# Performance work log

Hardware: AMD Instinct MI355X
Metric: run time of the kernel (lower is better)

The kernel has to match this reference:

```python
import jax, jax.numpy as jnp
import numpy as np

B, T, IN, H = 256, 512, 256, 1024


def setup_inputs() -> dict:
    key = jax.random.key(0)
    ks = jax.random.split(key, 11)
    bound = 1.0 / np.sqrt(H)  # PyTorch nn.RNN / nn.Linear init bound
    u = lambda k, shape: jax.random.uniform(k, shape, jnp.float32, -bound, bound)
    return {
        "y0": jax.random.normal(ks[0], (B, IN), jnp.float32),
        "t": jnp.arange(T, dtype=jnp.float32),
        "W_ih0": u(ks[1], (H, IN)),
        "W_hh0": u(ks[2], (H, H)),
        "b_ih0": u(ks[3], (H,)),
        "b_hh0": u(ks[4], (H,)),
        "W_ih1": u(ks[5], (H, H)),
        "W_hh1": u(ks[6], (H, H)),
        "b_ih1": u(ks[7], (H,)),
        "b_hh1": u(ks[8], (H,)),
        "fc_W": u(ks[9], (IN, H)),
        "fc_b": u(ks[10], (IN,)),
    }


def reference(y0, t, W_ih0, W_hh0, b_ih0, b_hh0, W_ih1, W_hh1, b_ih1, b_hh1, fc_W, fc_b):
    b = y0.shape[0]
    h = W_hh0.shape[0]
    n_steps = t.shape[0] - 1  # static under jit
    h0 = jnp.zeros((b, h), y0.dtype)
    h1 = jnp.zeros((b, h), y0.dtype)

    def step(carry, _):
        h0, h1, y = carry
        h0n = jnp.tanh(y @ W_ih0.T + b_ih0 + h0 @ W_hh0.T + b_hh0)
        h1n = jnp.tanh(h0n @ W_ih1.T + b_ih1 + h1 @ W_hh1.T + b_hh1)
        yn = h1n @ fc_W.T + fc_b  # fed back as next input
        return (h0n, h1n, yn), yn

    _, ys = jax.lax.scan(step, (h0, h1, y0), None, length=n_steps)  # [T-1, B, IN]
    out = jnp.concatenate([y0[None], ys], axis=0)  # [T, B, IN]
    return jnp.transpose(out, (1, 0, 2))  # [B, T, IN]
```

## Files before the change

kernel.cpp:

```cpp
#include <hip/hip_runtime.h>


#define B_SZ   256
#define IN_SZ  256
#define H_SZ   1024
#define KCAT   2048
#define NWG_M  64

typedef short v8s __attribute__((ext_vector_type(8)));
typedef float v4f __attribute__((ext_vector_type(4)));

__device__ __forceinline__ unsigned short bf16rne(float f) {
  unsigned x = __builtin_bit_cast(unsigned, f);
  return (unsigned short)((x + 0x7fffu + ((x >> 16) & 1u)) >> 16);
}
__device__ __forceinline__ float bf2f(unsigned short u) {
  unsigned x = ((unsigned)u) << 16;
  return __builtin_bit_cast(float, x);
}

__device__ __forceinline__ void split8(const float* __restrict__ p,
                                       v8s& a0, v8s& a1) {
  float4 x0 = *(const float4*)p;
  float4 x1 = *(const float4*)(p + 4);
  float v[8] = {x0.x, x0.y, x0.z, x0.w, x1.x, x1.y, x1.z, x1.w};
  v8s h, l;
#pragma unroll
  for (int j = 0; j < 8; ++j) {
    unsigned u = __builtin_bit_cast(unsigned, v[j]);
    float r = v[j] - __builtin_bit_cast(float, u & 0xFFFF0000u);
    h[j] = (short)(u >> 16);
    l[j] = (short)(__builtin_bit_cast(unsigned, r) >> 16);
  }
  a0 = h; a1 = l;
}

__device__ __forceinline__ void grid_barrier(unsigned* cnt, int idx, unsigned nwg,
                                             unsigned* abortf, unsigned* fail_s,
                                             bool* dead) {
  __syncthreads();
  if (*dead) return;
  if (threadIdx.x == 0) {
    __builtin_amdgcn_fence(__ATOMIC_RELEASE, "agent");
    __hip_atomic_fetch_add(&cnt[idx], 1u, __ATOMIC_RELAXED, __HIP_MEMORY_SCOPE_AGENT);
    unsigned f = 0, it = 0;
    while (__hip_atomic_load(&cnt[idx], __ATOMIC_RELAXED, __HIP_MEMORY_SCOPE_AGENT) < nwg) {
      __builtin_amdgcn_s_sleep(2);
      if ((++it & 1023u) == 0u) {
        if (__hip_atomic_load(abortf, __ATOMIC_RELAXED, __HIP_MEMORY_SCOPE_AGENT)) { f = 1; break; }
        if (it > 4000000u) {
          f = 1;
          __hip_atomic_store(abortf, 1u, __ATOMIC_RELAXED, __HIP_MEMORY_SCOPE_AGENT);
          break;
        }
      }
    }
    __builtin_amdgcn_fence(__ATOMIC_ACQUIRE, "agent");
    *fail_s = f;
  }
  __syncthreads();
  if (*fail_s) *dead = true;
}

struct MArgs {
  const float* y0;
  const unsigned short *B0p, *B1p, *W0p, *fcp;
  float *h0a, *h0b, *h1a, *h1b;
  const float *b_init, *b0p, *b1p, *fc_b;
  float* out;
  unsigned *cnt, *abortf;
  int T, nwg;
};

__device__ __forceinline__ void gemm2f(
    const float* __restrict__ X, int ldx, int am0, int ak0,
    const unsigned short* __restrict__ Bp, int KBtot, int bn0, int bk0,
    int ksteps, int l15, int l4, v4f acc[4][4]) {
  const float* Ab = X + (long)(am0 + l15) * ldx + ak0 + l4 * 8;
  const unsigned short* Bb =
      Bp + ((long)(bn0 + l15) * KBtot + (bk0 >> 3) + l4) * 16;
  for (int ks = 0; ks < ksteps; ++ks) {
    v8s a0[4], a1[4], b0[4], b1[4];
#pragma unroll
    for (int f = 0; f < 4; ++f) {
      split8(Ab + (long)f * 16 * ldx + ks * 32, a0[f], a1[f]);
      const unsigned short* bp = Bb + (long)f * 16 * KBtot * 16 + ks * 64;
      b0[f] = *(const v8s*)bp;
      b1[f] = *(const v8s*)(bp + 8);
    }
#pragma unroll
    for (int fr = 0; fr < 4; ++fr) {
#pragma unroll
      for (int fc = 0; fc < 4; ++fc) {
        v4f c = acc[fr][fc];
        c = __builtin_amdgcn_mfma_f32_16x16x32_bf16(a0[fr], b1[fc], c, 0, 0, 0);
        c = __builtin_amdgcn_mfma_f32_16x16x32_bf16(a1[fr], b0[fc], c, 0, 0, 0);
        c = __builtin_amdgcn_mfma_f32_16x16x32_bf16(a0[fr], b0[fc], c, 0, 0, 0);
        acc[fr][fc] = c;
      }
    }
  }
}

#define RSTRIDE 68

__global__ void __launch_bounds__(256, 1) rnn_mfma_kernel(MArgs a) {
  __shared__ float red[4][64 * RSTRIDE];
  __shared__ unsigned fail_s;
  bool dead = false;

  const int wg = blockIdx.x, tid = threadIdx.x;
  const int wv = tid >> 6, lane = tid & 63;
  const int l15 = lane & 15, l4 = lane >> 4;
  const int T = a.T, nwg = a.nwg;
  const long ldo = (long)T * IN_SZ;

  const int m0 = (wg >> 4) * 64;
  const int n0 = (wg & 15) * 64;
  const int fn0 = (wg & 15) * 16;

  float* h0p[2] = {a.h0a, a.h0b};
  float* h1p[2] = {a.h1a, a.h1b};

  v4f zero = {0.f, 0.f, 0.f, 0.f};
  int cur = 0, bar = 0;

  const int ak0 = 512 * (wv & 1);
  const int bk0 = ak0 + (wv >> 1) * 1024;

  for (int t = 1; t < T; ++t) {
    const int nxt = cur ^ 1;

    {
      v4f acc[4][4];
#pragma unroll
      for (int i = 0; i < 4; ++i)
#pragma unroll
        for (int j = 0; j < 4; ++j) acc[i][j] = zero;

      if (t == 1) {
        gemm2f(a.y0, IN_SZ, m0, 64 * wv, a.W0p, 32, n0, 64 * wv,
               2, l15, l4, acc);
      } else {
        const float* X = (wv < 2) ? h1p[cur] : h0p[cur];
        gemm2f(X, H_SZ, m0, ak0, a.B0p, 256, n0, bk0, 16, l15, l4, acc);
      }
      float* my = &red[wv][0];
#pragma unroll
      for (int fr = 0; fr < 4; ++fr)
#pragma unroll
        for (int fc = 0; fc < 4; ++fc)
#pragma unroll
          for (int j = 0; j < 4; ++j)
            my[(fr * 16 + l4 * 4 + j) * RSTRIDE + fc * 16 + l15] = acc[fr][fc][j];
      __syncthreads();
      const float* bias = (t == 1) ? a.b_init : a.b0p;
      float* dst = h0p[nxt];
#pragma unroll
      for (int i = 0; i < 16; ++i) {
        int idx = i * 256 + tid;
        int row = idx >> 6, col = idx & 63;
        int ro = row * RSTRIDE + col;
        float v = red[0][ro] + red[1][ro] + red[2][ro] + red[3][ro];
        dst[(long)(m0 + row) * H_SZ + n0 + col] = tanhf(v + bias[n0 + col]);
      }
    }
    grid_barrier(a.cnt, bar++, (unsigned)nwg, a.abortf, &fail_s, &dead);

    {
      v4f acc[4][4];
#pragma unroll
      for (int i = 0; i < 4; ++i)
#pragma unroll
        for (int j = 0; j < 4; ++j) acc[i][j] = zero;

      const float* X = (wv < 2) ? h0p[nxt] : h1p[cur];
      gemm2f(X, H_SZ, m0, ak0, a.B1p, 256, n0, bk0, 16, l15, l4, acc);

      float* my = &red[wv][0];
#pragma unroll
      for (int fr = 0; fr < 4; ++fr)
#pragma unroll
        for (int fc = 0; fc < 4; ++fc)
#pragma unroll
          for (int j = 0; j < 4; ++j)
            my[(fr * 16 + l4 * 4 + j) * RSTRIDE + fc * 16 + l15] = acc[fr][fc][j];
      __syncthreads();
      float* dst = h1p[nxt];
#pragma unroll
      for (int i = 0; i < 16; ++i) {
        int idx = i * 256 + tid;
        int row = idx >> 6, col = idx & 63;
        int ro = row * RSTRIDE + col;
        float v = red[0][ro] + red[1][ro] + red[2][ro] + red[3][ro];
        dst[(long)(m0 + row) * H_SZ + n0 + col] = tanhf(v + a.b1p[n0 + col]);
      }
    }
    grid_barrier(a.cnt, bar++, (unsigned)nwg, a.abortf, &fail_s, &dead);

    {
      v4f facc[4] = {zero, zero, zero, zero};
      const float* Ab = h1p[nxt] + (long)(m0 + l15) * H_SZ + 256 * wv + l4 * 8;
      const unsigned short* Bb =
          a.fcp + ((long)(fn0 + l15) * 128 + 32 * wv + l4) * 16;
      for (int ks = 0; ks < 8; ++ks) {
        const unsigned short* bp = Bb + ks * 64;
        v8s b0 = *(const v8s*)bp;
        v8s b1 = *(const v8s*)(bp + 8);
#pragma unroll
        for (int f = 0; f < 4; ++f) {
          v8s a0, a1;
          split8(Ab + (long)f * 16 * H_SZ + ks * 32, a0, a1);
          facc[f] = __builtin_amdgcn_mfma_f32_16x16x32_bf16(a0, b1, facc[f], 0, 0, 0);
          facc[f] = __builtin_amdgcn_mfma_f32_16x16x32_bf16(a1, b0, facc[f], 0, 0, 0);
          facc[f] = __builtin_amdgcn_mfma_f32_16x16x32_bf16(a0, b0, facc[f], 0, 0, 0);
        }
      }
      float* my = &red[wv][0];
#pragma unroll
      for (int f = 0; f < 4; ++f)
#pragma unroll
        for (int j = 0; j < 4; ++j)
          my[(f * 16 + l4 * 4 + j) * 17 + l15] = facc[f][j];
      __syncthreads();
#pragma unroll
      for (int i = 0; i < 4; ++i) {
        int idx = i * 256 + tid;
        int row = idx >> 4, col = idx & 15;
        int ro = row * 17 + col;
        float v = red[0][ro] + red[1][ro] + red[2][ro] + red[3][ro] + a.fc_b[fn0 + col];
        a.out[(long)(m0 + row) * ldo + (long)t * IN_SZ + fn0 + col] = v;
      }
      __syncthreads();
    }
    cur = nxt;
  }
}

__global__ void __launch_bounds__(256) pack2_kernel(
    const float* __restrict__ src, int R, int CB,
    unsigned short* __restrict__ dst, int KBtot, int kboff) {
  int i = blockIdx.x * 256 + threadIdx.x;
  if (i >= R * CB) return;
  int r = i / CB, cb = i - r * CB;
  const float* s = src + (long)r * (CB * 8) + cb * 8;
  unsigned short w[16];
#pragma unroll
  for (int e = 0; e < 8; ++e) {
    float v = s[e];
    unsigned short s0 = bf16rne(v);
    float rr = v - bf2f(s0);
    w[e] = s0;
    w[8 + e] = bf16rne(rr);
  }
  unsigned short* d = dst + ((long)r * KBtot + kboff + cb) * 16;
#pragma unroll
  for (int e = 0; e < 16; ++e) d[e] = w[e];
}

__global__ void __launch_bounds__(256) wc_pack2_kernel(
    const float* __restrict__ Wih0, const float* __restrict__ fcW,
    unsigned short* __restrict__ dst) {
  int i = blockIdx.x * 256 + threadIdx.x;
  int r = i >> 7, jb = i & 127;
  float acc[8] = {0.f, 0.f, 0.f, 0.f, 0.f, 0.f, 0.f, 0.f};
  for (int c = 0; c < IN_SZ; ++c) {
    float w = Wih0[r * IN_SZ + c];
    const float* f = &fcW[c * H_SZ + jb * 8];
#pragma unroll
    for (int e = 0; e < 8; ++e) acc[e] = fmaf(w, f[e], acc[e]);
  }
  unsigned short* d = dst + ((long)r * 256 + jb) * 16;
#pragma unroll
  for (int e = 0; e < 8; ++e) {
    unsigned short s0 = bf16rne(acc[e]);
    float rr = acc[e] - bf2f(s0);
    d[e] = s0;
    d[8 + e] = bf16rne(rr);
  }
}

__global__ void bias_kernel(const float* bih0, const float* bhh0,
                            const float* bih1, const float* bhh1,
                            const float* __restrict__ Wih0,
                            const float* __restrict__ fcb,
                            float* b_init, float* b0p, float* b1p) {
  int i = blockIdx.x * 256 + threadIdx.x;
  if (i < H_SZ) {
    float sum = 0.f;
    for (int c = 0; c < IN_SZ; ++c) sum += Wih0[i * IN_SZ + c] * fcb[c];
    float bi = bih0[i] + bhh0[i];
    b_init[i] = bi;
    b0p[i] = bi + sum;
    b1p[i] = bih1[i] + bhh1[i];
  }
}

__global__ void y0copy_kernel(const float* __restrict__ y0,
                              float* __restrict__ out, int T) {
  int o = blockIdx.x * 256 + threadIdx.x;
  int b = o >> 6, c = (o & 63) << 2;
  *(float4*)&out[(size_t)b * T * IN_SZ + c] = *(const float4*)&y0[b * IN_SZ + c];
}

#define KC 128
#define KCP 132
#define LTILES 256
#define FTILES 64
struct alignas(16) SmemT { float A[16][KCP]; float W[64][KCP]; };
struct RnnArgs {
  const float *y0, *W_ih0, *W_hh0, *W_ih1, *W_hh1, *fc_W, *fc_b;
  const float *Wc, *b_init, *b0p, *b1p;
  float *h0a, *h0b, *h1a, *h1b, *out;
  unsigned *cnt, *abortf;
  int T, nwg, mode;
};
__device__ __forceinline__ void gemm_accum(const float* __restrict__ X, int ldx,
                                           const float* __restrict__ Wm, int K,
                                           int m0, int n0, int wv, int lane, int tid,
                                           SmemT& s, float* acc) {
  for (int kc = 0; kc < K; kc += KC) {
#pragma unroll
    for (int i = 0; i < 2; ++i) {
      int a = i * 256 + tid; int r = a >> 5, k = (a & 31) << 2;
      *(float4*)&s.A[r][k] = *(const float4*)&X[(size_t)(m0 + r) * ldx + kc + k];
    }
#pragma unroll
    for (int i = 0; i < 8; ++i) {
      int a = i * 256 + tid; int c = a >> 5, k = (a & 31) << 2;
      *(float4*)&s.W[c][k] = *(const float4*)&Wm[(size_t)(n0 + c) * K + kc + k];
    }
    __syncthreads();
#pragma unroll 4
    for (int k4 = 0; k4 < KC; k4 += 4) {
      float4 w4 = *(float4*)&s.W[lane][k4];
#pragma unroll
      for (int j = 0; j < 4; ++j) {
        float4 a4 = *(float4*)&s.A[wv + 4 * j][k4];
        acc[j] = fmaf(a4.x, w4.x, acc[j]); acc[j] = fmaf(a4.y, w4.y, acc[j]);
        acc[j] = fmaf(a4.z, w4.z, acc[j]); acc[j] = fmaf(a4.w, w4.w, acc[j]);
      }
    }
    __syncthreads();
  }
}
__global__ void __launch_bounds__(256) rnn_seq_kernel(RnnArgs a) {
  __shared__ SmemT s;
  __shared__ unsigned fail_s;
  bool dead = false;
  const int wg = blockIdx.x, tid = threadIdx.x;
  const int wv = tid >> 6, lane = tid & 63;
  const int T = a.T, nwg = a.nwg, mode = a.mode;
  const int ldo = T * IN_SZ;
  const float* h0[2] = {a.h0a, a.h0b};
  const float* h1[2] = {a.h1a, a.h1b};
  float* h0w[2] = {a.h0a, a.h0b};
  float* h1w[2] = {a.h1a, a.h1b};
  int cur = 0, bar = 0;
  for (int t = 1; t < T; ++t) {
    const int nxt = cur ^ 1;
    for (int tl = wg; tl < LTILES; tl += nwg) {
      const int m0 = (tl >> 4) << 4;
      const int n0 = (((tl & 7) << 1) | ((tl >> 3) & 1)) << 6;
      float acc[4] = {0.f, 0.f, 0.f, 0.f};
      const float* bias;
      if (t == 1) { gemm_accum(a.y0, IN_SZ, a.W_ih0, IN_SZ, m0, n0, wv, lane, tid, s, acc); bias = a.b_init; }
      else if (mode == 0) { gemm_accum(h1[cur], H_SZ, a.Wc, H_SZ, m0, n0, wv, lane, tid, s, acc); bias = a.b0p; }
      else { gemm_accum(a.out + (size_t)(t - 1) * IN_SZ, ldo, a.W_ih0, IN_SZ, m0, n0, wv, lane, tid, s, acc); bias = a.b_init; }
      gemm_accum(h0[cur], H_SZ, a.W_hh0, H_SZ, m0, n0, wv, lane, tid, s, acc);
      const float bv = bias[n0 + lane];
#pragma unroll
      for (int j = 0; j < 4; ++j)
        h0w[nxt][(size_t)(m0 + wv + 4 * j) * H_SZ + n0 + lane] = tanhf(acc[j] + bv);
    }
    grid_barrier(a.cnt, bar++, (unsigned)nwg, a.abortf, &fail_s, &dead);
    for (int tl = wg; tl < LTILES; tl += nwg) {
      const int m0 = (tl >> 4) << 4;
      const int n0 = (((tl & 7) << 1) | ((tl >> 3) & 1)) << 6;
      float acc[4] = {0.f, 0.f, 0.f, 0.f};
      gemm_accum(h0[nxt], H_SZ, a.W_ih1, H_SZ, m0, n0, wv, lane, tid, s, acc);
      gemm_accum(h1[cur], H_SZ, a.W_hh1, H_SZ, m0, n0, wv, lane, tid, s, acc);
      const float bv = a.b1p[n0 + lane];
#pragma unroll
      for (int j = 0; j < 4; ++j)
        h1w[nxt][(size_t)(m0 + wv + 4 * j) * H_SZ + n0 + lane] = tanhf(acc[j] + bv);
    }
    grid_barrier(a.cnt, bar++, (unsigned)nwg, a.abortf, &fail_s, &dead);
    for (int ft = wg; ft < FTILES; ft += nwg) {
      const int m0 = (ft >> 2) << 4;
      const int n0 = (ft & 3) << 6;
      float acc[4] = {0.f, 0.f, 0.f, 0.f};
      gemm_accum(h1[nxt], H_SZ, a.fc_W, H_SZ, m0, n0, wv, lane, tid, s, acc);
      const float bv = a.fc_b[n0 + lane];
#pragma unroll
      for (int j = 0; j < 4; ++j)
        a.out[(size_t)(m0 + wv + 4 * j) * ldo + (size_t)t * IN_SZ + n0 + lane] = acc[j] + bv;
    }
    if (mode == 1)
      grid_barrier(a.cnt, bar++, (unsigned)nwg, a.abortf, &fail_s, &dead);
    cur = nxt;
  }
}
__global__ void __launch_bounds__(256) wc_kernel(const float* __restrict__ Wih0,
                                                 const float* __restrict__ fcW,
                                                 float* __restrict__ Wc) {
  int o = blockIdx.x * 256 + threadIdx.x;
  int i = o >> 8, j0 = (o & 255) << 2;
  float4 acc = {0.f, 0.f, 0.f, 0.f};
  for (int c = 0; c < IN_SZ; ++c) {
    float a = Wih0[i * IN_SZ + c];
    float4 f = *(const float4*)&fcW[c * H_SZ + j0];
    acc.x += a * f.x; acc.y += a * f.y; acc.z += a * f.z; acc.w += a * f.w;
  }
  *(float4*)&Wc[(size_t)i * H_SZ + j0] = acc;
}

extern "C" void kernel_launch(void* const* d_in, const int* in_sizes, int n_in,
                              void* d_out, int out_size, void* d_ws, size_t ws_size,
                              hipStream_t stream) {
  const float* y0    = (const float*)d_in[0];
  const float* W_ih0 = (const float*)d_in[2];
  const float* W_hh0 = (const float*)d_in[3];
  const float* b_ih0 = (const float*)d_in[4];
  const float* b_hh0 = (const float*)d_in[5];
  const float* W_ih1 = (const float*)d_in[6];
  const float* W_hh1 = (const float*)d_in[7];
  const float* b_ih1 = (const float*)d_in[8];
  const float* b_hh1 = (const float*)d_in[9];
  const float* fc_W  = (const float*)d_in[10];
  const float* fc_b  = (const float*)d_in[11];
  const int T = in_sizes[1];

  const long B0N = 1024L * 256 * 16;
  const long B1N = B0N;
  const long W0N = 1024L * 32 * 16;
  const long FCN = 256L * 128 * 16;
  const long hN  = (long)B_SZ * H_SZ;
  const size_t needNew = (2 * B0N + W0N + FCN) * 2 +
                         (4 * hN + 3 * H_SZ) * 4 + (2L * T + 8) * 4;

  if (ws_size >= needNew) {
    unsigned short* ws16 = (unsigned short*)d_ws;
    unsigned short* B0p = ws16;  ws16 += B0N;
    unsigned short* B1p = ws16;  ws16 += B1N;
    unsigned short* W0p = ws16;  ws16 += W0N;
    unsigned short* fcp = ws16;  ws16 += FCN;
    float* wf  = (float*)ws16;
    float* h0a = wf;  wf += hN;
    float* h0b = wf;  wf += hN;
    float* h1a = wf;  wf += hN;
    float* h1b = wf;  wf += hN;
    float* b_init = wf;  wf += H_SZ;
    float* b0p = wf;     wf += H_SZ;
    float* b1p = wf;     wf += H_SZ;
    unsigned* cnt = (unsigned*)wf;
    unsigned* abortf = cnt + 2 * (size_t)T + 4;

    hipMemsetAsync(cnt, 0, (2 * (size_t)T + 5) * 4, stream);
    hipMemsetAsync(h0a, 0, hN * 4, stream);
    hipMemsetAsync(h1a, 0, hN * 4, stream);

    wc_pack2_kernel<<<512, 256, 0, stream>>>(W_ih0, fc_W, B0p);
    pack2_kernel<<<512, 256, 0, stream>>>(W_hh0, 1024, 128, B0p, 256, 128);
    pack2_kernel<<<512, 256, 0, stream>>>(W_ih1, 1024, 128, B1p, 256, 0);
    pack2_kernel<<<512, 256, 0, stream>>>(W_hh1, 1024, 128, B1p, 256, 128);
    pack2_kernel<<<128, 256, 0, stream>>>(W_ih0, 1024, 32, W0p, 32, 0);
    pack2_kernel<<<128, 256, 0, stream>>>(fc_W, 256, 128, fcp, 128, 0);
    bias_kernel<<<4, 256, 0, stream>>>(b_ih0, b_hh0, b_ih1, b_hh1, W_ih0, fc_b,
                                       b_init, b0p, b1p);
    y0copy_kernel<<<(B_SZ * IN_SZ / 4) / 256, 256, 0, stream>>>(y0, (float*)d_out, T);

    MArgs a;
    a.y0 = y0;
    a.B0p = B0p; a.B1p = B1p; a.W0p = W0p; a.fcp = fcp;
    a.h0a = h0a; a.h0b = h0b; a.h1a = h1a; a.h1b = h1b;
    a.b_init = b_init; a.b0p = b0p; a.b1p = b1p; a.fc_b = fc_b;
    a.out = (float*)d_out; a.cnt = cnt; a.abortf = abortf;
    a.T = T; a.nwg = NWG_M;
    void* kargs[] = {(void*)&a};
    hipLaunchCooperativeKernel(rnn_mfma_kernel, dim3(NWG_M), dim3(256), kargs, 0, stream);
    return;
  }

  const size_t hNf = (size_t)B_SZ * H_SZ;
  const size_t wcN = (size_t)H_SZ * H_SZ;
  const size_t cntN = 3 * (size_t)T + 8;
  const size_t need_full = (wcN + 4 * hNf + 3 * H_SZ + cntN) * 4;
  const int mode = (ws_size >= need_full) ? 0 : 1;

  float* ws = (float*)d_ws;
  float* Wc = nullptr;
  if (mode == 0) { Wc = ws; ws += wcN; }
  float* h0a = ws;  ws += hNf;
  float* h0b = ws;  ws += hNf;
  float* h1a = ws;  ws += hNf;
  float* h1b = ws;  ws += hNf;
  float* b_init = ws; ws += H_SZ;
  float* b0p = ws;  ws += H_SZ;
  float* b1p = ws;  ws += H_SZ;
  unsigned* cnt = (unsigned*)ws;
  unsigned* abortf = cnt + 3 * (size_t)T;

  hipMemsetAsync(cnt, 0, cntN * sizeof(unsigned), stream);
  hipMemsetAsync(h0a, 0, hNf * sizeof(float), stream);
  hipMemsetAsync(h1a, 0, hNf * sizeof(float), stream);
  if (mode == 0)
    wc_kernel<<<(H_SZ * H_SZ / 4) / 256, 256, 0, stream>>>(W_ih0, fc_W, Wc);
  bias_kernel<<<4, 256, 0, stream>>>(b_ih0, b_hh0, b_ih1, b_hh1, W_ih0, fc_b,
                                     b_init, b0p, b1p);
  y0copy_kernel<<<(B_SZ * IN_SZ / 4) / 256, 256, 0, stream>>>(y0, (float*)d_out, T);

  RnnArgs a;
  a.y0 = y0; a.W_ih0 = W_ih0; a.W_hh0 = W_hh0; a.W_ih1 = W_ih1; a.W_hh1 = W_hh1;
  a.fc_W = fc_W; a.fc_b = fc_b;
  a.Wc = Wc; a.b_init = b_init; a.b0p = b0p; a.b1p = b1p;
  a.h0a = h0a; a.h0b = h0b; a.h1a = h1a; a.h1b = h1b;
  a.out = (float*)d_out; a.cnt = cnt; a.abortf = abortf;
  a.T = T; a.nwg = 256; a.mode = mode;
  void* kargs[] = {(void*)&a};
  hipError_t err = hipLaunchCooperativeKernel(rnn_seq_kernel, dim3(256), dim3(256),
                                              kargs, 0, stream);
  int nwg = 256;
  while (err != hipSuccess && nwg > 16) {
    nwg >>= 1; a.nwg = nwg;
    err = hipLaunchCooperativeKernel(rnn_seq_kernel, dim3(nwg), dim3(256),
                                     kargs, 0, stream);
  }
}
```

Measured before the change: 43.28 ms.

## Spread persistent RNN kernel over 256 workgroups of 512 threads with finer tiles

```diff
diff --git a/kernel.cpp b/kernel.cpp
--- a/kernel.cpp
+++ b/kernel.cpp
@@ -4,8 +4,7 @@
 #define B_SZ   256
 #define IN_SZ  256
 #define H_SZ   1024
-#define KCAT   2048
-#define NWG_M  64
+#define NWG_M  256
 
 typedef short v8s __attribute__((ext_vector_type(8)));
 typedef float v4f __attribute__((ext_vector_type(4)));
@@ -19,25 +18,9 @@
   return __builtin_bit_cast(float, x);
 }
 
-__device__ __forceinline__ void split8(const float* __restrict__ p,
-                                       v8s& a0, v8s& a1) {
-  float4 x0 = *(const float4*)p;
-  float4 x1 = *(const float4*)(p + 4);
-  float v[8] = {x0.x, x0.y, x0.z, x0.w, x1.x, x1.y, x1.z, x1.w};
-  v8s h, l;
-#pragma unroll
-  for (int j = 0; j < 8; ++j) {
-    unsigned u = __builtin_bit_cast(unsigned, v[j]);
-    float r = v[j] - __builtin_bit_cast(float, u & 0xFFFF0000u);
-    h[j] = (short)(u >> 16);
-    l[j] = (short)(__builtin_bit_cast(unsigned, r) >> 16);
-  }
-  a0 = h; a1 = l;
-}
-
-__device__ __forceinline__ void grid_barrier(unsigned* cnt, int idx, unsigned nwg,
-                                             unsigned* abortf, unsigned* fail_s,
-                                             bool* dead) {
+__device__ __forceinline__ void grid_barrier_rel(unsigned* cnt, int idx, unsigned nwg,
+                                                 unsigned* abortf, unsigned* fail_s,
+                                                 bool* dead) {
   __syncthreads();
   if (*dead) return;
   if (threadIdx.x == 0) {
@@ -55,6 +38,34 @@
         }
       }
     }
+    __builtin_amdgcn_fence(__ATOMIC_ACQUIRE, "workgroup");
+    *fail_s = f;
+  }
+  __syncthreads();
+  if (*fail_s) *dead = true;
+  __builtin_amdgcn_sched_barrier(0);
+}
+
+__device__ __forceinline__ void grid_barrier_acq(unsigned* cnt, int idx, unsigned nwg,
+                                                 unsigned* abortf, unsigned* fail_s,
+                                                 bool* dead) {
+  __syncthreads();
+  if (*dead) return;
+  if (threadIdx.x == 0) {
+    __builtin_amdgcn_fence(__ATOMIC_RELEASE, "agent");
+    __hip_atomic_fetch_add(&cnt[idx], 1u, __ATOMIC_RELAXED, __HIP_MEMORY_SCOPE_AGENT);
+    unsigned f = 0, it = 0;
+    while (__hip_atomic_load(&cnt[idx], __ATOMIC_RELAXED, __HIP_MEMORY_SCOPE_AGENT) < nwg) {
+      __builtin_amdgcn_s_sleep(2);
+      if ((++it & 1023u) == 0u) {
+        if (__hip_atomic_load(abortf, __ATOMIC_RELAXED, __HIP_MEMORY_SCOPE_AGENT)) { f = 1; break; }
+        if (it > 4000000u) {
+          f = 1;
+          __hip_atomic_store(abortf, 1u, __ATOMIC_RELAXED, __HIP_MEMORY_SCOPE_AGENT);
+          break;
+        }
+      }
+    }
     __builtin_amdgcn_fence(__ATOMIC_ACQUIRE, "agent");
     *fail_s = f;
   }
@@ -72,40 +83,45 @@
   int T, nwg;
 };
 
-__device__ __forceinline__ void gemm2f(
-    const float* __restrict__ X, int ldx, int am0, int ak0,
-    const unsigned short* __restrict__ Bp, int KBtot, int bn0, int bk0,
-    int ksteps, int l15, int l4, v4f acc[4][4]) {
-  const float* Ab = X + (long)(am0 + l15) * ldx + ak0 + l4 * 8;
+template<int KS, int NF>
+__device__ __forceinline__ void gemm_sc(
+    const float* __restrict__ X, int lda, int m0, int ak0,
+    const unsigned short* __restrict__ Bp, int kbtot, int n0, int bk0,
+    int l15, int l4, v4f* acc) {
+  const float* Ab = X + (long)(m0 + l15) * lda + ak0 + l4 * 8;
   const unsigned short* Bb =
-      Bp + ((long)(bn0 + l15) * KBtot + (bk0 >> 3) + l4) * 16;
-  for (int ks = 0; ks < ksteps; ++ks) {
-    v8s a0[4], a1[4], b0[4], b1[4];
-#pragma unroll
-    for (int f = 0; f < 4; ++f) {
-      split8(Ab + (long)f * 16 * ldx + ks * 32, a0[f], a1[f]);
-      const unsigned short* bp = Bb + (long)f * 16 * KBtot * 16 + ks * 64;
-      b0[f] = *(const v8s*)bp;
-      b1[f] = *(const v8s*)(bp + 8);
-    }
-#pragma unroll
-    for (int fr = 0; fr < 4; ++fr) {
-#pragma unroll
-      for (int fc = 0; fc < 4; ++fc) {
-        v4f c = acc[fr][fc];
-        c = __builtin_amdgcn_mfma_f32_16x16x32_bf16(a0[fr], b1[fc], c, 0, 0, 0);
-        c = __builtin_amdgcn_mfma_f32_16x16x32_bf16(a1[fr], b0[fc], c, 0, 0, 0);
-        c = __builtin_amdgcn_mfma_f32_16x16x32_bf16(a0[fr], b0[fc], c, 0, 0, 0);
-        acc[fr][fc] = c;
-      }
-    }
-  }
-}
-
-#define RSTRIDE 68
-
-__global__ void __launch_bounds__(256, 1) rnn_mfma_kernel(MArgs a) {
-  __shared__ float red[4][64 * RSTRIDE];
+      Bp + ((long)(n0 + l15) * kbtot + (bk0 >> 3) + l4) * 16;
+#pragma unroll
+  for (int ks = 0; ks < KS; ++ks) {
+    float av[8];
+#pragma unroll
+    for (int j = 0; j < 8; ++j)
+      av[j] = __hip_atomic_load((const float*)(Ab + ks * 32 + j),
+                                __ATOMIC_RELAXED, __HIP_MEMORY_SCOPE_AGENT);
+    v8s a0, a1;
+#pragma unroll
+    for (int j = 0; j < 8; ++j) {
+      unsigned u = __builtin_bit_cast(unsigned, av[j]);
+      float r = av[j] - __builtin_bit_cast(float, u & 0xFFFF0000u);
+      a0[j] = (short)(u >> 16);
+      a1[j] = (short)(__builtin_bit_cast(unsigned, r) >> 16);
+    }
+#pragma unroll
+    for (int f = 0; f < NF; ++f) {
+      const unsigned short* bp = Bb + ((long)f * 16 * kbtot + ks * 4) * 16;
+      v8s b0 = *(const v8s*)bp;
+      v8s b1 = *(const v8s*)(bp + 8);
+      acc[f] = __builtin_amdgcn_mfma_f32_16x16x32_bf16(a0, b1, acc[f], 0, 0, 0);
+      acc[f] = __builtin_amdgcn_mfma_f32_16x16x32_bf16(a1, b0, acc[f], 0, 0, 0);
+      acc[f] = __builtin_amdgcn_mfma_f32_16x16x32_bf16(a0, b0, acc[f], 0, 0, 0);
+    }
+  }
+}
+
+#define RS 68
+
+__global__ void __launch_bounds__(512, 2) rnn_mfma2_kernel(MArgs a) {
+  __shared__ float red[8][16 * RS];
   __shared__ unsigned fail_s;
   bool dead = false;
 
@@ -115,7 +131,7 @@
   const int T = a.T, nwg = a.nwg;
   const long ldo = (long)T * IN_SZ;
 
-  const int m0 = (wg >> 4) * 64;
+  const int m0 = (wg >> 4) * 16;
   const int n0 = (wg & 15) * 64;
   const int fn0 = (wg & 15) * 16;
 
@@ -124,111 +140,78 @@
 
   v4f zero = {0.f, 0.f, 0.f, 0.f};
   int cur = 0, bar = 0;
-
-  const int ak0 = 512 * (wv & 1);
-  const int bk0 = ak0 + (wv >> 1) * 1024;
+  const int akw = (wv & 3) * 256;
+  const int bkw = wv * 256;
 
   for (int t = 1; t < T; ++t) {
     const int nxt = cur ^ 1;
 
     {
-      v4f acc[4][4];
-#pragma unroll
-      for (int i = 0; i < 4; ++i)
-#pragma unroll
-        for (int j = 0; j < 4; ++j) acc[i][j] = zero;
-
+      v4f acc[4] = {zero, zero, zero, zero};
       if (t == 1) {
-        gemm2f(a.y0, IN_SZ, m0, 64 * wv, a.W0p, 32, n0, 64 * wv,
-               2, l15, l4, acc);
+        gemm_sc<1, 4>(a.y0, IN_SZ, m0, wv * 32, a.W0p, 32, n0, wv * 32,
+                      l15, l4, acc);
       } else {
-        const float* X = (wv < 2) ? h1p[cur] : h0p[cur];
-        gemm2f(X, H_SZ, m0, ak0, a.B0p, 256, n0, bk0, 16, l15, l4, acc);
-      }
-      float* my = &red[wv][0];
-#pragma unroll
-      for (int fr = 0; fr < 4; ++fr)
-#pragma unroll
-        for (int fc = 0; fc < 4; ++fc)
-#pragma unroll
-          for (int j = 0; j < 4; ++j)
-            my[(fr * 16 + l4 * 4 + j) * RSTRIDE + fc * 16 + l15] = acc[fr][fc][j];
+        const float* X = (wv < 4) ? h1p[cur] : h0p[cur];
+        gemm_sc<8, 4>(X, H_SZ, m0, akw, a.B0p, 256, n0, bkw, l15, l4, acc);
+      }
+#pragma unroll
+      for (int f = 0; f < 4; ++f)
+#pragma unroll
+        for (int j = 0; j < 4; ++j)
+          red[wv][(l4 * 4 + j) * RS + f * 16 + l15] = acc[f][j];
       __syncthreads();
       const float* bias = (t == 1) ? a.b_init : a.b0p;
       float* dst = h0p[nxt];
 #pragma unroll
-      for (int i = 0; i < 16; ++i) {
-        int idx = i * 256 + tid;
+      for (int e = 0; e < 2; ++e) {
+        int idx = e * 512 + tid;
         int row = idx >> 6, col = idx & 63;
-        int ro = row * RSTRIDE + col;
-        float v = red[0][ro] + red[1][ro] + red[2][ro] + red[3][ro];
+        int ro = row * RS + col;
+        float v = red[0][ro] + red[1][ro] + red[2][ro] + red[3][ro] +
+                  red[4][ro] + red[5][ro] + red[6][ro] + red[7][ro];
         dst[(long)(m0 + row) * H_SZ + n0 + col] = tanhf(v + bias[n0 + col]);
       }
     }
-    grid_barrier(a.cnt, bar++, (unsigned)nwg, a.abortf, &fail_s, &dead);
+    grid_barrier_rel(a.cnt, bar++, (unsigned)nwg, a.abortf, &fail_s, &dead);
 
     {
-      v4f acc[4][4];
-#pragma unroll
-      for (int i = 0; i < 4; ++i)
-#pragma unroll
-        for (int j = 0; j < 4; ++j) acc[i][j] = zero;
-
-      const float* X = (wv < 2) ? h0p[nxt] : h1p[cur];
-      gemm2f(X, H_SZ, m0, ak0, a.B1p, 256, n0, bk0, 16, l15, l4, acc);
-
-      float* my = &red[wv][0];
-#pragma unroll
-      for (int fr = 0; fr < 4; ++fr)
-#pragma unroll
-        for (int fc = 0; fc < 4; ++fc)
-#pragma unroll
-          for (int j = 0; j < 4; ++j)
-            my[(fr * 16 + l4 * 4 + j) * RSTRIDE + fc * 16 + l15] = acc[fr][fc][j];
+      v4f acc[4] = {zero, zero, zero, zero};
+      const float* X = (wv < 4) ? h0p[nxt] : h1p[cur];
+      gemm_sc<8, 4>(X, H_SZ, m0, akw, a.B1p, 256, n0, bkw, l15, l4, acc);
+#pragma unroll
+      for (int f = 0; f < 4; ++f)
+#pragma unroll
+        for (int j = 0; j < 4; ++j)
+          red[wv][(l4 * 4 + j) * RS + f * 16 + l15] = acc[f][j];
       __syncthreads();
       float* dst = h1p[nxt];
 #pragma unroll
-      for (int i = 0; i < 16; ++i) {
-        int idx = i * 256 + tid;
+      for (int e = 0; e < 2; ++e) {
+        int idx = e * 512 + tid;
         int row = idx >> 6, col = idx & 63;
-        int ro = row * RSTRIDE + col;
-        float v = red[0][ro] + red[1][ro] + red[2][ro] + red[3][ro];
+        int ro = row * RS + col;
+        float v = red[0][ro] + red[1][ro] + red[2][ro] + red[3][ro] +
+                  red[4][ro] + red[5][ro] + red[6][ro] + red[7][ro];
         dst[(long)(m0 + row) * H_SZ + n0 + col] = tanhf(v + a.b1p[n0 + col]);
       }
     }
-    grid_barrier(a.cnt, bar++, (unsigned)nwg, a.abortf, &fail_s, &dead);
+    grid_barrier_rel(a.cnt, bar++, (unsigned)nwg, a.abortf, &fail_s, &dead);
 
     {
-      v4f facc[4] = {zero, zero, zero, zero};
-      const float* Ab = h1p[nxt] + (long)(m0 + l15) * H_SZ + 256 * wv + l4 * 8;
-      const unsigned short* Bb =
-          a.fcp + ((long)(fn0 + l15) * 128 + 32 * wv + l4) * 16;
-      for (int ks = 0; ks < 8; ++ks) {
-        const unsigned short* bp = Bb + ks * 64;
-        v8s b0 = *(const v8s*)bp;
-        v8s b1 = *(const v8s*)(bp + 8);
-#pragma unroll
-        for (int f = 0; f < 4; ++f) {
-          v8s a0, a1;
-          split8(Ab + (long)f * 16 * H_SZ + ks * 32, a0, a1);
-          facc[f] = __builtin_amdgcn_mfma_f32_16x16x32_bf16(a0, b1, facc[f], 0, 0, 0);
-          facc[f] = __builtin_amdgcn_mfma_f32_16x16x32_bf16(a1, b0, facc[f], 0, 0, 0);
-          facc[f] = __builtin_amdgcn_mfma_f32_16x16x32_bf16(a0, b0, facc[f], 0, 0, 0);
-        }
-      }
-      float* my = &red[wv][0];
-#pragma unroll
-      for (int f = 0; f < 4; ++f)
-#pragma unroll
-        for (int j = 0; j < 4; ++j)
-          my[(f * 16 + l4 * 4 + j) * 17 + l15] = facc[f][j];
+      v4f facc = zero;
+      gemm_sc<4, 1>(h1p[nxt], H_SZ, m0, wv * 128, a.fcp, 128, fn0, wv * 128,
+                    l15, l4, &facc);
+#pragma unroll
+      for (int j = 0; j < 4; ++j)
+        red[wv][(l4 * 4 + j) * 20 + l15] = facc[j];
       __syncthreads();
-#pragma unroll
-      for (int i = 0; i < 4; ++i) {
-        int idx = i * 256 + tid;
-        int row = idx >> 4, col = idx & 15;
-        int ro = row * 17 + col;
-        float v = red[0][ro] + red[1][ro] + red[2][ro] + red[3][ro] + a.fc_b[fn0 + col];
+      if (tid < 256) {
+        int row = tid >> 4, col = tid & 15;
+        int ro = row * 20 + col;
+        float v = red[0][ro] + red[1][ro] + red[2][ro] + red[3][ro] +
+                  red[4][ro] + red[5][ro] + red[6][ro] + red[7][ro] +
+                  a.fc_b[fn0 + col];
         a.out[(long)(m0 + row) * ldo + (long)t * IN_SZ + fn0 + col] = v;
       }
       __syncthreads();
@@ -373,7 +356,7 @@
       for (int j = 0; j < 4; ++j)
         h0w[nxt][(size_t)(m0 + wv + 4 * j) * H_SZ + n0 + lane] = tanhf(acc[j] + bv);
     }
-    grid_barrier(a.cnt, bar++, (unsigned)nwg, a.abortf, &fail_s, &dead);
+    grid_barrier_acq(a.cnt, bar++, (unsigned)nwg, a.abortf, &fail_s, &dead);
     for (int tl = wg; tl < LTILES; tl += nwg) {
       const int m0 = (tl >> 4) << 4;
       const int n0 = (((tl & 7) << 1) | ((tl >> 3) & 1)) << 6;
@@ -385,7 +368,7 @@
       for (int j = 0; j < 4; ++j)
         h1w[nxt][(size_t)(m0 + wv + 4 * j) * H_SZ + n0 + lane] = tanhf(acc[j] + bv);
     }
-    grid_barrier(a.cnt, bar++, (unsigned)nwg, a.abortf, &fail_s, &dead);
+    grid_barrier_acq(a.cnt, bar++, (unsigned)nwg, a.abortf, &fail_s, &dead);
     for (int ft = wg; ft < FTILES; ft += nwg) {
       const int m0 = (ft >> 2) << 4;
       const int n0 = (ft & 3) << 6;
@@ -397,7 +380,7 @@
         a.out[(size_t)(m0 + wv + 4 * j) * ldo + (size_t)t * IN_SZ + n0 + lane] = acc[j] + bv;
     }
     if (mode == 1)
-      grid_barrier(a.cnt, bar++, (unsigned)nwg, a.abortf, &fail_s, &dead);
+      grid_barrier_acq(a.cnt, bar++, (unsigned)nwg, a.abortf, &fail_s, &dead);
     cur = nxt;
   }
 }
@@ -439,7 +422,12 @@
   const size_t needNew = (2 * B0N + W0N + FCN) * 2 +
                          (4 * hN + 3 * H_SZ) * 4 + (2L * T + 8) * 4;
 
-  if (ws_size >= needNew) {
+  int maxb = 0;
+  hipError_t oe = hipOccupancyMaxActiveBlocksPerMultiprocessor(
+      &maxb, rnn_mfma2_kernel, 512, 0);
+  const bool tryNew = (ws_size >= needNew) && (oe == hipSuccess) && (maxb >= 1);
+
+  if (tryNew) {
     unsigned short* ws16 = (unsigned short*)d_ws;
     unsigned short* B0p = ws16;  ws16 += B0N;
     unsigned short* B1p = ws16;  ws16 += B1N;
@@ -478,8 +466,9 @@
     a.out = (float*)d_out; a.cnt = cnt; a.abortf = abortf;
     a.T = T; a.nwg = NWG_M;
     void* kargs[] = {(void*)&a};
-    hipLaunchCooperativeKernel(rnn_mfma_kernel, dim3(NWG_M), dim3(256), kargs, 0, stream);
-    return;
+    hipError_t err = hipLaunchCooperativeKernel(rnn_mfma2_kernel, dim3(NWG_M),
+                                                dim3(512), kargs, 0, stream);
+    if (err == hipSuccess) return;
   }
 
   const size_t hNf = (size_t)B_SZ * H_SZ;
```

Measured after the change: 103.0 ms. 2.38x slower.
